# Optimization experiments

Hardware: AMD Instinct MI355X
Metric: run time of the kernel (lower is better)

Reference implementation:

```python
import jax, jax.numpy as jnp
import numpy as np

D_MODEL = 1024
N_HEADS = 4
KEY_DIM = 1024   # expand_k=1.0
VALUE_DIM = 2048 # expand_v=2.0
DK = KEY_DIM // N_HEADS    # 256
DV = VALUE_DIM // N_HEADS  # 512
LOW_RANK = 16
GATE_NORM = 16.0
EPS = 1e-5


def setup_inputs() -> dict:
    key = jax.random.key(0)
    ks = jax.random.split(key, 10)
    B, L = 2, 2048
    gain = 2.0 ** (-2.5)

    def xavier(k, shape, g=gain):
        fan_in, fan_out = shape[0], shape[1]
        a = g * np.sqrt(6.0 / (fan_in + fan_out))
        return jax.random.uniform(k, shape, jnp.float32, -a, a)

    return {
        "x": jax.random.normal(ks[0], (B, L, D_MODEL), jnp.float32),
        "Wq": xavier(ks[1], (D_MODEL, KEY_DIM)),
        "Wk": xavier(ks[2], (D_MODEL, KEY_DIM)),
        "Wv": xavier(ks[3], (D_MODEL, VALUE_DIM)),
        "Wg": xavier(ks[4], (D_MODEL, VALUE_DIM)),
        "gk_w1": xavier(ks[5], (D_MODEL, LOW_RANK)),
        "gk_w2": xavier(ks[6], (LOW_RANK, KEY_DIM)),
        "gk_b2": jnp.zeros((KEY_DIM,), jnp.float32),
        "g_norm_w": jnp.ones((DV,), jnp.float32),
        "Wo": xavier(ks[7], (VALUE_DIM, D_MODEL)),
    }


def _gla_scan(q, k, v, gk):
    # q,k: [B,H,L,Dk]; v: [B,H,L,Dv]; gk: [B,H,L,Dk] (log decay)
    # recurrence: S_t = diag(exp(gk_t)) S_{t-1} + k_t v_t^T ; o_t = q_t S_t
    B, H, L, dk = q.shape
    dv = v.shape[-1]
    # time-major for scan
    qs = jnp.moveaxis(q, 2, 0)
    ks_ = jnp.moveaxis(k, 2, 0)
    vs = jnp.moveaxis(v, 2, 0)
    gs = jnp.moveaxis(gk, 2, 0)

    def step(S, inp):
        q_t, k_t, v_t, g_t = inp  # [B,H,Dk], [B,H,Dk], [B,H,Dv], [B,H,Dk]
        S = S * jnp.exp(g_t)[..., None] + k_t[..., None] * v_t[..., None, :]
        o_t = jnp.einsum('bhk,bhkv->bhv', q_t, S)
        return S, o_t

    S0 = jnp.zeros((B, H, dk, dv), q.dtype)
    _, os = jax.lax.scan(step, S0, (qs, ks_, vs, gs))
    return jnp.moveaxis(os, 0, 2)  # [B,H,L,Dv]


def reference(x, Wq, Wk, Wv, Wg, gk_w1, gk_w2, gk_b2, g_norm_w, Wo):
    B, L, _ = x.shape
    scale = DK ** -0.5

    def heads(t, d):
        return t.reshape(B, L, N_HEADS, d).transpose(0, 2, 1, 3)  # b h l d

    q = heads(x @ Wq, DK) * scale
    k = heads(x @ Wk, DK)
    v = heads(x @ Wv, DV)
    gk = heads(jax.nn.log_sigmoid((x @ gk_w1) @ gk_w2 + gk_b2) / GATE_NORM, DK)

    o = _gla_scan(q, k, v, gk)                 # [B,H,L,Dv]
    o = o.transpose(0, 2, 1, 3)                # [B,L,H,Dv]

    g = (x @ Wg).reshape(B, L, N_HEADS, DV)
    # FusedRMSNormSwishGate: RMSNorm(o) * silu(g)
    rms = o * jax.lax.rsqrt(jnp.mean(o * o, axis=-1, keepdims=True) + EPS)
    o = (rms * g_norm_w) * (g * jax.nn.sigmoid(g))
    o = o.reshape(B, L, VALUE_DIM)
    return o @ Wo
```

## Files before the change

### kernel.cpp

```cpp
#include <hip/hip_runtime.h>
#include <hip/hip_bf16.h>
#include <math.h>

#define NHEADS 4
#define DKH 256
#define DVH 512
#define SEQL 2048
#define NB 2
#define NTOK (NB*SEQL)
#define DM 1024
#define KDT 1024
#define VDT 2048
#define CHUNK 128
#define NCH (SEQL/CHUNK)

typedef unsigned short u16;
typedef unsigned int   u32;
typedef unsigned long long u64;
typedef __attribute__((ext_vector_type(8))) short bf16x8;
typedef __attribute__((ext_vector_type(4))) float f32x4;

__device__ inline u16 f2bf(float f) {
  __hip_bfloat16 h = __float2bfloat16(f);
  return *reinterpret_cast<u16*>(&h);
}
__device__ inline float bf2f(u16 u) {
  u32 x = ((u32)u) << 16;
  return __uint_as_float(x);
}

__device__ __forceinline__ void gload16(const u16* g, u16* l) {
  __builtin_amdgcn_global_load_lds(
      (const __attribute__((address_space(1))) u32*)g,
      (__attribute__((address_space(3))) u32*)l,
      16, 0, 0);
}

__global__ __launch_bounds__(256)
void f2bf_kernel(const float* __restrict__ in, u16* __restrict__ out, int n)
{
  const int i = (blockIdx.x * 256 + threadIdx.x) * 8;
  if (i >= n) return;
  const float4 x0 = *(const float4*)&in[i];
  const float4 x1 = *(const float4*)&in[i + 4];
  int4 p;
  p.x = f2bf(x0.x) | ((u32)f2bf(x0.y) << 16);
  p.y = f2bf(x0.z) | ((u32)f2bf(x0.w) << 16);
  p.z = f2bf(x1.x) | ((u32)f2bf(x1.y) << 16);
  p.w = f2bf(x1.z) | ((u32)f2bf(x1.w) << 16);
  *(int4*)&out[i] = p;
}

__global__ __launch_bounds__(256)
void transpose_f2bf(const float* __restrict__ W, u16* __restrict__ Wt, int K, int N)
{
  __shared__ float Ts[64][69];
  const int n0 = blockIdx.x * 64, k0 = blockIdx.y * 64;
  const int tx = threadIdx.x & 15, ty = threadIdx.x >> 4;
  #pragma unroll
  for (int r = 0; r < 4; ++r) {
    const int k = ty + r * 16;
    const float4 w4 = *(const float4*)&W[(size_t)(k0 + k) * N + n0 + tx * 4];
    Ts[tx*4 + 0][k] = w4.x;
    Ts[tx*4 + 1][k] = w4.y;
    Ts[tx*4 + 2][k] = w4.z;
    Ts[tx*4 + 3][k] = w4.w;
  }
  __syncthreads();
  #pragma unroll
  for (int r = 0; r < 4; ++r) {
    const int n = ty + r * 16;
    u64 pk = (u64)f2bf(Ts[n][tx*4 + 0]) | ((u64)f2bf(Ts[n][tx*4 + 1]) << 16)
           | ((u64)f2bf(Ts[n][tx*4 + 2]) << 32) | ((u64)f2bf(Ts[n][tx*4 + 3]) << 48);
    *(u64*)&Wt[(size_t)(n0 + n) * K + k0 + tx * 4] = pk;
  }
}

__global__ __launch_bounds__(256)
void gemm_qkvg(const u16* __restrict__ A, const u16* __restrict__ Wall,
               u16* __restrict__ Qh, u16* __restrict__ Kh,
               u16* __restrict__ Vt, u16* __restrict__ Gh, float qscale)
{
  __shared__ __align__(16) u16 As[2][128 * 32];
  __shared__ __align__(16) u16 Bs[2][128 * 32];
  const int tid = threadIdx.x;
  const int lane = tid & 63, wave = tid >> 6;
  const int wr = wave >> 1, wc = wave & 1;
  const int l15 = lane & 15, l4 = lane >> 4;
  const int bx = blockIdx.x;
  const int bm = blockIdx.y * 128, bn = bx * 128;

  f32x4 acc[4][4];
  #pragma unroll
  for (int i = 0; i < 4; ++i)
    #pragma unroll
    for (int j = 0; j < 4; ++j)
      acc[i][j] = (f32x4){0.f, 0.f, 0.f, 0.f};

  const int sRow = wave * 32 + (lane >> 2);
  const int sCol = (lane & 3) * 8;
  const u16* Ag0 = &A   [(size_t)(bm + sRow) * DM + sCol];
  const u16* Ag1 = &A   [(size_t)(bm + sRow + 16) * DM + sCol];
  const u16* Bg0 = &Wall[(size_t)(bn + sRow) * DM + sCol];
  const u16* Bg1 = &Wall[(size_t)(bn + sRow + 16) * DM + sCol];
  const int lb0 = (wave * 32) * 32, lb1 = (wave * 32 + 16) * 32;

  gload16(Ag0, &As[0][lb0]);
  gload16(Ag1, &As[0][lb1]);
  gload16(Bg0, &Bs[0][lb0]);
  gload16(Bg1, &Bs[0][lb1]);
  __syncthreads();

  for (int k0 = 0; k0 < DM; k0 += 32) {
    const int cur = (k0 >> 5) & 1;
    if (k0 + 32 < DM) {
      gload16(Ag0 + k0 + 32, &As[cur ^ 1][lb0]);
      gload16(Ag1 + k0 + 32, &As[cur ^ 1][lb1]);
      gload16(Bg0 + k0 + 32, &Bs[cur ^ 1][lb0]);
      gload16(Bg1 + k0 + 32, &Bs[cur ^ 1][lb1]);
    }
    bf16x8 af[4], bfv[4];
    #pragma unroll
    for (int mi = 0; mi < 4; ++mi)
      af[mi] = *(const bf16x8*)&As[cur][(wr*64 + mi*16 + l15) * 32 + l4*8];
    #pragma unroll
    for (int ni = 0; ni < 4; ++ni)
      bfv[ni] = *(const bf16x8*)&Bs[cur][(wc*64 + ni*16 + l15) * 32 + l4*8];
    #pragma unroll
    for (int mi = 0; mi < 4; ++mi)
      #pragma unroll
      for (int ni = 0; ni < 4; ++ni)
        acc[mi][ni] = __builtin_amdgcn_mfma_f32_16x16x32_bf16(af[mi], bfv[ni], acc[mi][ni], 0, 0, 0);
    __syncthreads();
  }

  if (bx < 8) {
    #pragma unroll
    for (int mi = 0; mi < 4; ++mi)
      #pragma unroll
      for (int ni = 0; ni < 4; ++ni) {
        const int col = bn + wc*64 + ni*16 + l15;
        #pragma unroll
        for (int r = 0; r < 4; ++r)
          Qh[(size_t)(bm + wr*64 + mi*16 + l4*4 + r) * 1024 + col] = f2bf(acc[mi][ni][r] * qscale);
      }
  } else if (bx < 16) {
    #pragma unroll
    for (int mi = 0; mi < 4; ++mi)
      #pragma unroll
      for (int ni = 0; ni < 4; ++ni) {
        const int col = bn - 1024 + wc*64 + ni*16 + l15;
        #pragma unroll
        for (int r = 0; r < 4; ++r)
          Kh[(size_t)(bm + wr*64 + mi*16 + l4*4 + r) * 1024 + col] = f2bf(acc[mi][ni][r]);
      }
  } else if (bx < 32) {
    #pragma unroll
    for (int mi = 0; mi < 4; ++mi) {
      const int row0 = bm + wr*64 + mi*16 + l4*4;
      const int b = row0 >> 11, l = row0 & 2047;
      #pragma unroll
      for (int ni = 0; ni < 4; ++ni) {
        const int colV = bn - 2048 + wc*64 + ni*16 + l15;
        const int h = colV >> 9, dv = colV & 511;
        u64 pk = (u64)f2bf(acc[mi][ni][0]) | ((u64)f2bf(acc[mi][ni][1]) << 16)
               | ((u64)f2bf(acc[mi][ni][2]) << 32) | ((u64)f2bf(acc[mi][ni][3]) << 48);
        *(u64*)&Vt[((size_t)((b*4 + h)*512 + dv)) * SEQL + l] = pk;
      }
    }
  } else {
    #pragma unroll
    for (int mi = 0; mi < 4; ++mi)
      #pragma unroll
      for (int ni = 0; ni < 4; ++ni) {
        const int col = bn - 4096 + wc*64 + ni*16 + l15;
        #pragma unroll
        for (int r = 0; r < 4; ++r)
          Gh[(size_t)(bm + wr*64 + mi*16 + l4*4 + r) * 2048 + col] = f2bf(acc[mi][ni][r]);
      }
  }
}

__global__ __launch_bounds__(256)
void gemm_bf16(const u16* __restrict__ A, const u16* __restrict__ Bt,
               float* __restrict__ C, int M, int N, int K, float scale)
{
  __shared__ __align__(16) u16 As[2][128 * 32];
  __shared__ __align__(16) u16 Bs[2][128 * 32];
  const int tid = threadIdx.x;
  const int lane = tid & 63, wave = tid >> 6;
  const int wr = wave >> 1, wc = wave & 1;
  const int l15 = lane & 15, l4 = lane >> 4;
  const int bm = blockIdx.y * 128, bn = blockIdx.x * 128;

  f32x4 acc[4][4];
  #pragma unroll
  for (int i = 0; i < 4; ++i)
    #pragma unroll
    for (int j = 0; j < 4; ++j)
      acc[i][j] = (f32x4){0.f, 0.f, 0.f, 0.f};

  const int sRow = wave * 32 + (lane >> 2);
  const int sCol = (lane & 3) * 8;
  const u16* Ag0 = &A [(size_t)(bm + sRow) * K + sCol];
  const u16* Ag1 = &A [(size_t)(bm + sRow + 16) * K + sCol];
  const u16* Bg0 = &Bt[(size_t)(bn + sRow) * K + sCol];
  const u16* Bg1 = &Bt[(size_t)(bn + sRow + 16) * K + sCol];
  const int lb0 = (wave * 32) * 32, lb1 = (wave * 32 + 16) * 32;

  gload16(Ag0, &As[0][lb0]);
  gload16(Ag1, &As[0][lb1]);
  gload16(Bg0, &Bs[0][lb0]);
  gload16(Bg1, &Bs[0][lb1]);
  __syncthreads();

  for (int k0 = 0; k0 < K; k0 += 32) {
    const int cur = (k0 >> 5) & 1;
    if (k0 + 32 < K) {
      gload16(Ag0 + k0 + 32, &As[cur ^ 1][lb0]);
      gload16(Ag1 + k0 + 32, &As[cur ^ 1][lb1]);
      gload16(Bg0 + k0 + 32, &Bs[cur ^ 1][lb0]);
      gload16(Bg1 + k0 + 32, &Bs[cur ^ 1][lb1]);
    }
    bf16x8 af[4], bfv[4];
    #pragma unroll
    for (int mi = 0; mi < 4; ++mi)
      af[mi] = *(const bf16x8*)&As[cur][(wr*64 + mi*16 + l15) * 32 + l4*8];
    #pragma unroll
    for (int ni = 0; ni < 4; ++ni)
      bfv[ni] = *(const bf16x8*)&Bs[cur][(wc*64 + ni*16 + l15) * 32 + l4*8];
    #pragma unroll
    for (int mi = 0; mi < 4; ++mi)
      #pragma unroll
      for (int ni = 0; ni < 4; ++ni)
        acc[mi][ni] = __builtin_amdgcn_mfma_f32_16x16x32_bf16(af[mi], bfv[ni], acc[mi][ni], 0, 0, 0);
    __syncthreads();
  }

  #pragma unroll
  for (int mi = 0; mi < 4; ++mi)
    #pragma unroll
    for (int ni = 0; ni < 4; ++ni) {
      const int col = bn + wc*64 + ni*16 + l15;
      #pragma unroll
      for (int r = 0; r < 4; ++r) {
        const int row = bm + wr*64 + mi*16 + l4*4 + r;
        C[(size_t)row * N + col] = acc[mi][ni][r] * scale;
      }
    }
}

__global__ __launch_bounds__(256)
void gemm_u(const float* __restrict__ X, const float* __restrict__ W1,
            float* __restrict__ U)
{
  __shared__ float Xs[64][65];
  __shared__ __align__(16) float W1s[64][16];
  const int tid = threadIdx.x;
  const int row0 = blockIdx.x * 64;
  const int rr = tid & 63, gg = tid >> 6;
  float acc[4] = {0.f, 0.f, 0.f, 0.f};
  for (int k0 = 0; k0 < DM; k0 += 64) {
    #pragma unroll
    for (int rep = 0; rep < 4; ++rep) {
      const int m = (tid >> 4) + rep * 16;
      const int kk = (tid & 15) << 2;
      const float4 x4 = *(const float4*)&X[(size_t)(row0 + m) * DM + k0 + kk];
      Xs[kk+0][m] = x4.x; Xs[kk+1][m] = x4.y; Xs[kk+2][m] = x4.z; Xs[kk+3][m] = x4.w;
    }
    {
      const int kk = tid >> 2, n = (tid & 3) << 2;
      *(float4*)&W1s[kk][n] = *(const float4*)&W1[(size_t)(k0 + kk) * 16 + n];
    }
    __syncthreads();
    #pragma unroll
    for (int k2 = 0; k2 < 64; ++k2) {
      const float xv = Xs[k2][rr];
      const float4 w4 = *(const float4*)&W1s[k2][gg << 2];
      acc[0] += xv * w4.x; acc[1] += xv * w4.y; acc[2] += xv * w4.z; acc[3] += xv * w4.w;
    }
    __syncthreads();
  }
  *(float4*)&U[(size_t)(row0 + rr) * 16 + (gg << 2)] =
      make_float4(acc[0], acc[1], acc[2], acc[3]);
}

__device__ inline float ls_exp(float z) {
  const float ls = (z >= 0.f) ? -log1pf(expf(-z)) : (z - log1pf(expf(z)));
  return expf(ls * 0.0625f);
}

__global__ __launch_bounds__(256)
void gate_kernel(const float* __restrict__ U, const float* __restrict__ W2,
                 const float* __restrict__ b2, float* __restrict__ EGKo)
{
  __shared__ float Us[16];
  const int row = blockIdx.x, tid = threadIdx.x;
  if (tid < 16) Us[tid] = U[row * 16 + tid];
  __syncthreads();
  const int d0 = tid << 2;
  float4 z = *(const float4*)&b2[d0];
  #pragma unroll
  for (int r = 0; r < 16; ++r) {
    const float u = Us[r];
    const float4 w4 = *(const float4*)&W2[r * 1024 + d0];
    z.x += u * w4.x; z.y += u * w4.y; z.z += u * w4.z; z.w += u * w4.w;
  }
  float4 e = make_float4(ls_exp(z.x), ls_exp(z.y), ls_exp(z.z), ls_exp(z.w));
  *(float4*)&EGKo[(size_t)row * 1024 + d0] = e;
}

__global__ __launch_bounds__(256)
void chunk_prep(const u16* __restrict__ Qh, const u16* __restrict__ Kh,
                const float* __restrict__ EG, u16* __restrict__ qtb,
                u16* __restrict__ ktb, u16* __restrict__ khb,
                float* __restrict__ lamC)
{
  const int j = blockIdx.x;
  const int bh = blockIdx.y;
  const int b = bh >> 2, h = bh & 3;
  const int tid = threadIdx.x;
  const size_t base = ((size_t)(b * SEQL + j * CHUNK)) * KDT + h * DKH + tid;
  float cum = 1.f;
  for (int t = 0; t < CHUNK; t += 4) {
    const size_t i0 = base + (size_t)t * KDT;
    float d[4], q[4], k[4];
    #pragma unroll
    for (int u = 0; u < 4; ++u) {
      d[u] = EG[i0 + (size_t)u * KDT];
      q[u] = bf2f(Qh[i0 + (size_t)u * KDT]);
      k[u] = bf2f(Kh[i0 + (size_t)u * KDT]);
    }
    #pragma unroll
    for (int u = 0; u < 4; ++u) {
      cum *= d[u];
      qtb[i0 + (size_t)u * KDT] = f2bf(q[u] * cum);
      ktb[i0 + (size_t)u * KDT] = f2bf(k[u] / cum);
    }
  }
  lamC[(bh * NCH + j) * 256 + tid] = cum;
  for (int t = 0; t < CHUNK; t += 4) {
    const size_t i0 = base + (size_t)t * KDT;
    u16 kt4[4];
    #pragma unroll
    for (int u = 0; u < 4; ++u) kt4[u] = ktb[i0 + (size_t)u * KDT];
    #pragma unroll
    for (int u = 0; u < 4; ++u)
      khb[i0 + (size_t)u * KDT] = f2bf(bf2f(kt4[u]) * cum);
  }
}

__global__ __launch_bounds__(256)
void gla_pstate_mfma(const u16* __restrict__ kh, const u16* __restrict__ Vt,
                     float* __restrict__ P)
{
  const int mb = blockIdx.x, nb = blockIdx.y, jc = blockIdx.z;
  const int bh = jc >> 4, j = jc & 15;
  const int b = bh >> 2, h = bh & 3;
  const int tid = threadIdx.x;
  const int lane = tid & 63, wave = tid >> 6;
  const int wr = wave >> 1, wc = wave & 1;
  const int l15 = lane & 15, l4 = lane >> 4;
  const int tok0 = b * SEQL + j * CHUNK;

  __shared__ __align__(16) u16 Al[128 * 40];
  __shared__ __align__(16) u16 Blt[128 * 40];

  f32x4 acc[4][4];
  #pragma unroll
  for (int i = 0; i < 4; ++i)
    #pragma unroll
    for (int jj = 0; jj < 4; ++jj) acc[i][jj] = (f32x4){0.f,0.f,0.f,0.f};

  for (int kt0 = 0; kt0 < CHUNK; kt0 += 32) {
    {
      const int srow = tid >> 2, scol = (tid & 3) * 8;
      *(int4*)&Al[(srow)    * 40 + scol] =
        *(const int4*)&Vt[((size_t)(bh*512 + mb*128 + srow))    * SEQL + j*CHUNK + kt0 + scol];
      *(int4*)&Al[(64+srow) * 40 + scol] =
        *(const int4*)&Vt[((size_t)(bh*512 + mb*128 + 64+srow)) * SEQL + j*CHUNK + kt0 + scol];
    }
    {
      const int t = tid & 31;
      #pragma unroll
      for (int i = 0; i < 2; ++i) {
        const int dkg = (tid >> 5) * 16 + i * 8;
        int4 v = *(const int4*)&kh[(size_t)(tok0 + kt0 + t) * KDT + h*DKH + nb*128 + dkg];
        const u16* pv = (const u16*)&v;
        #pragma unroll
        for (int u = 0; u < 8; ++u) Blt[(dkg + u)*40 + t] = pv[u];
      }
    }
    __syncthreads();
    bf16x8 af[4], bv[4];
    #pragma unroll
    for (int mi = 0; mi < 4; ++mi)
      af[mi] = *(const bf16x8*)&Al[(wr*64 + mi*16 + l15)*40 + l4*8];
    #pragma unroll
    for (int ni = 0; ni < 4; ++ni)
      bv[ni] = *(const bf16x8*)&Blt[(wc*64 + ni*16 + l15)*40 + l4*8];
    #pragma unroll
    for (int mi = 0; mi < 4; ++mi)
      #pragma unroll
      for (int ni = 0; ni < 4; ++ni)
        acc[mi][ni] = __builtin_amdgcn_mfma_f32_16x16x32_bf16(af[mi], bv[ni], acc[mi][ni], 0, 0, 0);
    __syncthreads();
  }

  #pragma unroll
  for (int mi = 0; mi < 4; ++mi)
    #pragma unroll
    for (int ni = 0; ni < 4; ++ni) {
      const int col = nb*128 + wc*64 + ni*16 + l15;
      #pragma unroll
      for (int r = 0; r < 4; ++r) {
        const int row = mb*128 + wr*64 + mi*16 + l4*4 + r;
        P[(size_t)jc * 131072 + (size_t)row * 256 + col] = acc[mi][ni][r];
      }
    }
}

__global__ __launch_bounds__(256)
void gla_sscan(const float* __restrict__ P, const float* __restrict__ lamC,
               u16* __restrict__ SjT)
{
  const int bh = blockIdx.y;
  const int e0 = blockIdx.x * 1024 + threadIdx.x * 4;
  const int dv = e0 >> 8, dk = e0 & 255;
  float4 S = make_float4(0.f, 0.f, 0.f, 0.f);
  for (int j = 0; j < NCH; ++j) {
    const size_t cb = (size_t)(bh * NCH + j);
    const float4 lam = *(const float4*)&lamC[cb * 256 + dk];
    const size_t idx = cb * 131072 + (size_t)dv * 256 + dk;
    const float4 tmp = *(const float4*)&P[idx];
    u64 pk = (u64)f2bf(S.x) | ((u64)f2bf(S.y) << 16)
           | ((u64)f2bf(S.z) << 32) | ((u64)f2bf(S.w) << 48);
    *(u64*)&SjT[idx] = pk;
    S.x = lam.x * S.x + tmp.x;
    S.y = lam.y * S.y + tmp.y;
    S.z = lam.z * S.z + tmp.z;
    S.w = lam.w * S.w + tmp.w;
  }
}

__global__ __launch_bounds__(256)
void gla_intra_mfma(const u16* __restrict__ qt, const u16* __restrict__ kt,
                    const u16* __restrict__ Vt, const u16* __restrict__ SjT,
                    float* __restrict__ O)
{
  const int half = blockIdx.x;
  const int j    = blockIdx.y;
  const int bh   = blockIdx.z;
  const int b = bh >> 2, h = bh & 3;
  const int tid = threadIdx.x;
  const int lane = tid & 63, wave = tid >> 6;
  const int wr = wave >> 1, wc = wave & 1;
  const int l15 = lane & 15, l4 = lane >> 4;
  const int tok0 = b * SEQL + j * CHUNK;

  __shared__ __align__(16) u16 Pl[128 * 136];
  __shared__ __align__(16) u16 stg[128 * 136];
  u16* As = stg;
  u16* Bs = stg + 128 * 40;

  const size_t qkBase = (size_t)tok0 * KDT + h * DKH;
  const size_t sjBase = (size_t)(bh * NCH + j) * 131072;

  const int srow = tid >> 2;
  const int scol = (tid & 3) * 8;

  f32x4 acc[4][4];
  #pragma unroll
  for (int i = 0; i < 4; ++i)
    #pragma unroll
    for (int jj = 0; jj < 4; ++jj) acc[i][jj] = (f32x4){0.f,0.f,0.f,0.f};

  int4 ra0 = *(const int4*)&qt[qkBase + (size_t)srow      * KDT + scol];
  int4 ra1 = *(const int4*)&qt[qkBase + (size_t)(64+srow) * KDT + scol];
  int4 rb0 = *(const int4*)&kt[qkBase + (size_t)srow      * KDT + scol];
  int4 rb1 = *(const int4*)&kt[qkBase + (size_t)(64+srow) * KDT + scol];

  for (int dk0 = 0; dk0 < DKH; dk0 += 32) {
    __syncthreads();
    *(int4*)&As[(srow)    * 40 + scol] = ra0;
    *(int4*)&As[(64+srow) * 40 + scol] = ra1;
    *(int4*)&Bs[(srow)    * 40 + scol] = rb0;
    *(int4*)&Bs[(64+srow) * 40 + scol] = rb1;
    __syncthreads();
    if (dk0 + 32 < DKH) {
      ra0 = *(const int4*)&qt[qkBase + (size_t)srow      * KDT + dk0 + 32 + scol];
      ra1 = *(const int4*)&qt[qkBase + (size_t)(64+srow) * KDT + dk0 + 32 + scol];
      rb0 = *(const int4*)&kt[qkBase + (size_t)srow      * KDT + dk0 + 32 + scol];
      rb1 = *(const int4*)&kt[qkBase + (size_t)(64+srow) * KDT + dk0 + 32 + scol];
    }
    bf16x8 af[4], bv[4];
    #pragma unroll
    for (int mi = 0; mi < 4; ++mi)
      af[mi] = *(const bf16x8*)&As[(wr*64 + mi*16 + l15) * 40 + l4*8];
    #pragma unroll
    for (int ni = 0; ni < 4; ++ni)
      bv[ni] = *(const bf16x8*)&Bs[(wc*64 + ni*16 + l15) * 40 + l4*8];
    #pragma unroll
    for (int mi = 0; mi < 4; ++mi)
      #pragma unroll
      for (int ni = 0; ni < 4; ++ni)
        acc[mi][ni] = __builtin_amdgcn_mfma_f32_16x16x32_bf16(af[mi], bv[ni], acc[mi][ni], 0, 0, 0);
  }
  __syncthreads();

  #pragma unroll
  for (int mi = 0; mi < 4; ++mi)
    #pragma unroll
    for (int ni = 0; ni < 4; ++ni) {
      const int s = wc*64 + ni*16 + l15;
      #pragma unroll
      for (int r = 0; r < 4; ++r) {
        const int t = wr*64 + mi*16 + l4*4 + r;
        Pl[t*136 + s] = (s <= t) ? f2bf(acc[mi][ni][r]) : (u16)0;
      }
    }
  __syncthreads();

  for (int dt = 0; dt < 2; ++dt) {
    const int dvBase = half*256 + dt*128;
    f32x4 acc2[4][4];
    #pragma unroll
    for (int i = 0; i < 4; ++i)
      #pragma unroll
      for (int jj = 0; jj < 4; ++jj) acc2[i][jj] = (f32x4){0.f,0.f,0.f,0.f};

    int4 ia0 = *(const int4*)&qt [qkBase + (size_t)srow      * KDT + scol];
    int4 ia1 = *(const int4*)&qt [qkBase + (size_t)(64+srow) * KDT + scol];
    int4 ib0 = *(const int4*)&SjT[sjBase + (size_t)(dvBase + srow)      * 256 + scol];
    int4 ib1 = *(const int4*)&SjT[sjBase + (size_t)(dvBase + 64 + srow) * 256 + scol];

    for (int k0 = 0; k0 < DKH; k0 += 32) {
      __syncthreads();
      *(int4*)&As[(srow)    * 40 + scol] = ia0;
      *(int4*)&As[(64+srow) * 40 + scol] = ia1;
      *(int4*)&Bs[(srow)    * 40 + scol] = ib0;
      *(int4*)&Bs[(64+srow) * 40 + scol] = ib1;
      __syncthreads();
      if (k0 + 32 < DKH) {
        ia0 = *(const int4*)&qt [qkBase + (size_t)srow      * KDT + k0 + 32 + scol];
        ia1 = *(const int4*)&qt [qkBase + (size_t)(64+srow) * KDT + k0 + 32 + scol];
        ib0 = *(const int4*)&SjT[sjBase + (size_t)(dvBase + srow)      * 256 + k0 + 32 + scol];
        ib1 = *(const int4*)&SjT[sjBase + (size_t)(dvBase + 64 + srow) * 256 + k0 + 32 + scol];
      }
      bf16x8 af[4], bv[4];
      #pragma unroll
      for (int mi = 0; mi < 4; ++mi)
        af[mi] = *(const bf16x8*)&As[(wr*64 + mi*16 + l15) * 40 + l4*8];
      #pragma unroll
      for (int ni = 0; ni < 4; ++ni)
        bv[ni] = *(const bf16x8*)&Bs[(wc*64 + ni*16 + l15) * 40 + l4*8];
      #pragma unroll
      for (int mi = 0; mi < 4; ++mi)
        #pragma unroll
        for (int ni = 0; ni < 4; ++ni)
          acc2[mi][ni] = __builtin_amdgcn_mfma_f32_16x16x32_bf16(af[mi], bv[ni], acc2[mi][ni], 0, 0, 0);
    }
    __syncthreads();

    #pragma unroll
    for (int i = 0; i < 8; ++i) {
      const int row = i*16 + (tid >> 4);
      const int col8 = (tid & 15) * 8;
      *(int4*)&stg[row*136 + col8] =
        *(const int4*)&Vt[((size_t)(bh*512 + dvBase + row)) * SEQL + j*CHUNK + col8];
    }
    __syncthreads();
    #pragma unroll
    for (int ks = 0; ks < 4; ++ks) {
      bf16x8 af2[4], bv2[4];
      #pragma unroll
      for (int mi = 0; mi < 4; ++mi)
        af2[mi] = *(const bf16x8*)&Pl[(wr*64 + mi*16 + l15)*136 + ks*32 + l4*8];
      #pragma unroll
      for (int ni = 0; ni < 4; ++ni)
        bv2[ni] = *(const bf16x8*)&stg[(wc*64 + ni*16 + l15)*136 + ks*32 + l4*8];
      #pragma unroll
      for (int mi = 0; mi < 4; ++mi)
        #pragma unroll
        for (int ni = 0; ni < 4; ++ni)
          acc2[mi][ni] = __builtin_amdgcn_mfma_f32_16x16x32_bf16(af2[mi], bv2[ni], acc2[mi][ni], 0, 0, 0);
    }
    #pragma unroll
    for (int mi = 0; mi < 4; ++mi)
      #pragma unroll
      for (int ni = 0; ni < 4; ++ni) {
        const int col = h*DVH + dvBase + wc*64 + ni*16 + l15;
        #pragma unroll
        for (int r = 0; r < 4; ++r) {
          const int row = tok0 + wr*64 + mi*16 + l4*4 + r;
          O[(size_t)row * VDT + col] = acc2[mi][ni][r];
        }
      }
    __syncthreads();
  }
}

__global__ __launch_bounds__(256)
void epilogue(const float* __restrict__ O, const u16* __restrict__ G,
              const float* __restrict__ w, u16* __restrict__ Y)
{
  const int row = blockIdx.x;
  const int tid = threadIdx.x;
  __shared__ float sred[4];
  for (int h = 0; h < NHEADS; ++h) {
    const size_t base = (size_t)row * VDT + h * DVH;
    const float2 o2 = *(const float2*)&O[base + tid * 2];
    float ss = o2.x * o2.x + o2.y * o2.y;
    #pragma unroll
    for (int off = 32; off > 0; off >>= 1) ss += __shfl_down(ss, off);
    if ((tid & 63) == 0) sred[tid >> 6] = ss;
    __syncthreads();
    const float tot = sred[0] + sred[1] + sred[2] + sred[3];
    const float rs = rsqrtf(tot * (1.f / DVH) + 1e-5f);
    const u32 g2p = *(const u32*)&G[base + tid * 2];
    const float gx = bf2f((u16)(g2p & 0xffff));
    const float gy = bf2f((u16)(g2p >> 16));
    const float2 w2 = *(const float2*)&w[tid * 2];
    const float y0 = o2.x * rs * w2.x * gx / (1.f + expf(-gx));
    const float y1 = o2.y * rs * w2.y * gy / (1.f + expf(-gy));
    const u32 pk = (u32)f2bf(y0) | ((u32)f2bf(y1) << 16);
    *(u32*)&Y[base + tid * 2] = pk;
    __syncthreads();
  }
}

extern "C" void kernel_launch(void* const* d_in, const int* in_sizes, int n_in,
                              void* d_out, int out_size, void* d_ws, size_t ws_size,
                              hipStream_t stream)
{
  const float* x    = (const float*)d_in[0];
  const float* Wq   = (const float*)d_in[1];
  const float* Wk   = (const float*)d_in[2];
  const float* Wv   = (const float*)d_in[3];
  const float* Wg   = (const float*)d_in[4];
  const float* gw1  = (const float*)d_in[5];
  const float* gw2  = (const float*)d_in[6];
  const float* gb2  = (const float*)d_in[7];
  const float* gnw  = (const float*)d_in[8];
  const float* Wo   = (const float*)d_in[9];
  float* out = (float*)d_out;

  float* ws = (float*)d_ws;
  const size_t M = 1024ull * 1024ull;
  u16*   Qbh  = (u16*)(ws);
  u16*   Kbh  = (u16*)(ws + 2*M);
  float* EGK  = ws + 4*M;
  u16*   Vtb  = (u16*)(ws + 8*M);
  u16*   qtb  = (u16*)(ws + 12*M);
  u16*   ktb  = (u16*)(ws + 14*M);
  u16*   Gbh  = (u16*)(ws + 16*M);
  float* Ob   = ws + 20*M;
  float* Sjb  = ws + 28*M;
  float* lamC = ws + 44*M;
  float* Ub   = ws + 44*M + 32768;
  u16*   khb  = (u16*)(ws + 45*M);
  u16*   xb   = (u16*)(ws + 47*M);
  u16*   Wallb= (u16*)(ws + 49*M);
  u16*   Wob  = (u16*)(ws + 52*M);
  u16*   SjTb = (u16*)(ws + 53*M);
  u16*   Y2b  = (u16*)(ws);

  const float qscale = 0.0625f;

  f2bf_kernel  <<<2048, 256, 0, stream>>>(x, xb, NTOK * DM);
  transpose_f2bf<<<dim3(16, 16), 256, 0, stream>>>(Wq, Wallb,                1024, 1024);
  transpose_f2bf<<<dim3(16, 16), 256, 0, stream>>>(Wk, Wallb + 1024*1024,    1024, 1024);
  transpose_f2bf<<<dim3(32, 16), 256, 0, stream>>>(Wv, Wallb + 2048*1024,    1024, 2048);
  transpose_f2bf<<<dim3(32, 16), 256, 0, stream>>>(Wg, Wallb + 4096ull*1024, 1024, 2048);
  transpose_f2bf<<<dim3(16, 32), 256, 0, stream>>>(Wo, Wob, 2048, 1024);

  gemm_qkvg<<<dim3(48, 32), 256, 0, stream>>>(xb, Wallb, Qbh, Kbh, Vtb, Gbh, qscale);
  gemm_u      <<<64, 256, 0, stream>>>(x, gw1, Ub);
  gate_kernel <<<NTOK, 256, 0, stream>>>(Ub, gw2, gb2, EGK);

  chunk_prep<<<dim3(NCH, 8), 256, 0, stream>>>(Qbh, Kbh, EGK, qtb, ktb, khb, lamC);

  gla_pstate_mfma<<<dim3(4, 2, 128), 256, 0, stream>>>(khb, Vtb, Sjb);
  gla_sscan      <<<dim3(128, 8), 256, 0, stream>>>(Sjb, lamC, SjTb);
  gla_intra_mfma <<<dim3(2, NCH, 8), 256, 0, stream>>>(qtb, ktb, Vtb, SjTb, Ob);

  epilogue<<<NTOK, 256, 0, stream>>>(Ob, Gbh, gnw, Y2b);
  gemm_bf16<<<dim3(8, 32), 256, 0, stream>>>(Y2b, Wob, out, NTOK, 1024, 2048, 1.f);
}
```

Measured before the change: 301.3 us.

## Widen QKVG GEMM tile to 128x256 with swizzle and fuse intra q·S passes

The fused QKVG projection GEMM moves from 128x128 to 128x256 tiles, so each wave holds 4x8 accumulators and the grid halves. A block-index remap groups tiles that share A rows. In the intra-chunk kernel, the two q·S_j inter-chunk products for both 128-wide dv halves are now computed in one k-loop that shares the q tile, rather than reloading q for each half. This halves redundant q loads and raises MFMA work per LDS read, at the cost of roughly double accumulator registers, which may lower occupancy or cause spills.

```diff
diff --git a/kernel.cpp b/kernel.cpp
--- a/kernel.cpp
+++ b/kernel.cpp
@@ -82,86 +82,94 @@
                u16* __restrict__ Vt, u16* __restrict__ Gh, float qscale)
 {
   __shared__ __align__(16) u16 As[2][128 * 32];
-  __shared__ __align__(16) u16 Bs[2][128 * 32];
+  __shared__ __align__(16) u16 Bs[2][256 * 32];
   const int tid = threadIdx.x;
   const int lane = tid & 63, wave = tid >> 6;
   const int wr = wave >> 1, wc = wave & 1;
   const int l15 = lane & 15, l4 = lane >> 4;
-  const int bx = blockIdx.x;
-  const int bm = blockIdx.y * 128, bn = bx * 128;
-
-  f32x4 acc[4][4];
+
+  const int flat = blockIdx.y * 24 + blockIdx.x;
+  const int nf = (flat & 7) * 96 + (flat >> 3);
+  const int bx = nf % 24, by = nf / 24;
+  const int bm = by * 128, bn = bx * 256;
+
+  f32x4 acc[4][8];
   #pragma unroll
   for (int i = 0; i < 4; ++i)
     #pragma unroll
-    for (int j = 0; j < 4; ++j)
+    for (int j = 0; j < 8; ++j)
       acc[i][j] = (f32x4){0.f, 0.f, 0.f, 0.f};
 
-  const int sRow = wave * 32 + (lane >> 2);
-  const int sCol = (lane & 3) * 8;
-  const u16* Ag0 = &A   [(size_t)(bm + sRow) * DM + sCol];
-  const u16* Ag1 = &A   [(size_t)(bm + sRow + 16) * DM + sCol];
-  const u16* Bg0 = &Wall[(size_t)(bn + sRow) * DM + sCol];
-  const u16* Bg1 = &Wall[(size_t)(bn + sRow + 16) * DM + sCol];
-  const int lb0 = (wave * 32) * 32, lb1 = (wave * 32 + 16) * 32;
-
-  gload16(Ag0, &As[0][lb0]);
-  gload16(Ag1, &As[0][lb1]);
-  gload16(Bg0, &Bs[0][lb0]);
-  gload16(Bg1, &Bs[0][lb1]);
+  const int sR = lane >> 2;
+  const int sC = (lane & 3) * 8;
+  const u16* Ag0 = &A[(size_t)(bm + wave*32 + sR) * DM + sC];
+  const u16* Ag1 = &A[(size_t)(bm + wave*32 + 16 + sR) * DM + sC];
+  const u16* Bg[4];
+  #pragma unroll
+  for (int q = 0; q < 4; ++q)
+    Bg[q] = &Wall[(size_t)(bn + wave*64 + q*16 + sR) * DM + sC];
+  const int la0 = (wave*32) * 32, la1 = (wave*32 + 16) * 32;
+  int lb[4];
+  #pragma unroll
+  for (int q = 0; q < 4; ++q) lb[q] = (wave*64 + q*16) * 32;
+
+  gload16(Ag0, &As[0][la0]);
+  gload16(Ag1, &As[0][la1]);
+  #pragma unroll
+  for (int q = 0; q < 4; ++q) gload16(Bg[q], &Bs[0][lb[q]]);
   __syncthreads();
 
   for (int k0 = 0; k0 < DM; k0 += 32) {
     const int cur = (k0 >> 5) & 1;
     if (k0 + 32 < DM) {
-      gload16(Ag0 + k0 + 32, &As[cur ^ 1][lb0]);
-      gload16(Ag1 + k0 + 32, &As[cur ^ 1][lb1]);
-      gload16(Bg0 + k0 + 32, &Bs[cur ^ 1][lb0]);
-      gload16(Bg1 + k0 + 32, &Bs[cur ^ 1][lb1]);
-    }
-    bf16x8 af[4], bfv[4];
+      gload16(Ag0 + k0 + 32, &As[cur ^ 1][la0]);
+      gload16(Ag1 + k0 + 32, &As[cur ^ 1][la1]);
+      #pragma unroll
+      for (int q = 0; q < 4; ++q) gload16(Bg[q] + k0 + 32, &Bs[cur ^ 1][lb[q]]);
+    }
+    bf16x8 af[4], bfv[8];
     #pragma unroll
     for (int mi = 0; mi < 4; ++mi)
       af[mi] = *(const bf16x8*)&As[cur][(wr*64 + mi*16 + l15) * 32 + l4*8];
     #pragma unroll
-    for (int ni = 0; ni < 4; ++ni)
-      bfv[ni] = *(const bf16x8*)&Bs[cur][(wc*64 + ni*16 + l15) * 32 + l4*8];
-    #pragma unroll
-    for (int mi = 0; mi < 4; ++mi)
-      #pragma unroll
-      for (int ni = 0; ni < 4; ++ni)
+    for (int ni = 0; ni < 8; ++ni)
+      bfv[ni] = *(const bf16x8*)&Bs[cur][(wc*128 + ni*16 + l15) * 32 + l4*8];
+    #pragma unroll
+    for (int mi = 0; mi < 4; ++mi)
+      #pragma unroll
+      for (int ni = 0; ni < 8; ++ni)
         acc[mi][ni] = __builtin_amdgcn_mfma_f32_16x16x32_bf16(af[mi], bfv[ni], acc[mi][ni], 0, 0, 0);
     __syncthreads();
   }
 
-  if (bx < 8) {
-    #pragma unroll
-    for (int mi = 0; mi < 4; ++mi)
-      #pragma unroll
-      for (int ni = 0; ni < 4; ++ni) {
-        const int col = bn + wc*64 + ni*16 + l15;
+  if (bx < 4) {
+    #pragma unroll
+    for (int mi = 0; mi < 4; ++mi)
+      #pragma unroll
+      for (int ni = 0; ni < 8; ++ni) {
+        const int col = bn + wc*128 + ni*16 + l15;
         #pragma unroll
         for (int r = 0; r < 4; ++r)
           Qh[(size_t)(bm + wr*64 + mi*16 + l4*4 + r) * 1024 + col] = f2bf(acc[mi][ni][r] * qscale);
       }
-  } else if (bx < 16) {
-    #pragma unroll
-    for (int mi = 0; mi < 4; ++mi)
-      #pragma unroll
-      for (int ni = 0; ni < 4; ++ni) {
-        const int col = bn - 1024 + wc*64 + ni*16 + l15;
+  } else if (bx < 8) {
+    #pragma unroll
+    for (int mi = 0; mi < 4; ++mi)
+      #pragma unroll
+      for (int ni = 0; ni < 8; ++ni) {
+        const int col = bn - 1024 + wc*128 + ni*16 + l15;
         #pragma unroll
         for (int r = 0; r < 4; ++r)
           Kh[(size_t)(bm + wr*64 + mi*16 + l4*4 + r) * 1024 + col] = f2bf(acc[mi][ni][r]);
       }
-  } else if (bx < 32) {
+  } else if (bx < 16) {
     #pragma unroll
     for (int mi = 0; mi < 4; ++mi) {
       const int row0 = bm + wr*64 + mi*16 + l4*4;
       const int b = row0 >> 11, l = row0 & 2047;
       #pragma unroll
-      for (int ni = 0; ni < 4; ++ni) {
-        const int colV = bn - 2048 + wc*64 + ni*16 + l15;
+      for (int ni = 0; ni < 8; ++ni) {
+        const int colV = bn - 2048 + wc*128 + ni*16 + l15;
         const int h = colV >> 9, dv = colV & 511;
         u64 pk = (u64)f2bf(acc[mi][ni][0]) | ((u64)f2bf(acc[mi][ni][1]) << 16)
                | ((u64)f2bf(acc[mi][ni][2]) << 32) | ((u64)f2bf(acc[mi][ni][3]) << 48);
@@ -172,8 +180,8 @@
     #pragma unroll
     for (int mi = 0; mi < 4; ++mi)
       #pragma unroll
-      for (int ni = 0; ni < 4; ++ni) {
-        const int col = bn - 4096 + wc*64 + ni*16 + l15;
+      for (int ni = 0; ni < 8; ++ni) {
+        const int col = bn - 4096 + wc*128 + ni*16 + l15;
         #pragma unroll
         for (int r = 0; r < 4; ++r)
           Gh[(size_t)(bm + wr*64 + mi*16 + l4*4 + r) * 2048 + col] = f2bf(acc[mi][ni][r]);
@@ -460,8 +468,9 @@
 
   __shared__ __align__(16) u16 Pl[128 * 136];
   __shared__ __align__(16) u16 stg[128 * 136];
-  u16* As = stg;
-  u16* Bs = stg + 128 * 40;
+  u16* As  = stg;
+  u16* Bs0 = stg + 128 * 40;
+  u16* Bs1 = stg + 2 * 128 * 40;
 
   const size_t qkBase = (size_t)tok0 * KDT + h * DKH;
   const size_t sjBase = (size_t)(bh * NCH + j) * 131072;
@@ -482,10 +491,10 @@
 
   for (int dk0 = 0; dk0 < DKH; dk0 += 32) {
     __syncthreads();
-    *(int4*)&As[(srow)    * 40 + scol] = ra0;
-    *(int4*)&As[(64+srow) * 40 + scol] = ra1;
-    *(int4*)&Bs[(srow)    * 40 + scol] = rb0;
-    *(int4*)&Bs[(64+srow) * 40 + scol] = rb1;
+    *(int4*)&As [(srow)    * 40 + scol] = ra0;
+    *(int4*)&As [(64+srow) * 40 + scol] = ra1;
+    *(int4*)&Bs0[(srow)    * 40 + scol] = rb0;
+    *(int4*)&Bs0[(64+srow) * 40 + scol] = rb1;
     __syncthreads();
     if (dk0 + 32 < DKH) {
       ra0 = *(const int4*)&qt[qkBase + (size_t)srow      * KDT + dk0 + 32 + scol];
@@ -499,7 +508,7 @@
       af[mi] = *(const bf16x8*)&As[(wr*64 + mi*16 + l15) * 40 + l4*8];
     #pragma unroll
     for (int ni = 0; ni < 4; ++ni)
-      bv[ni] = *(const bf16x8*)&Bs[(wc*64 + ni*16 + l15) * 40 + l4*8];
+      bv[ni] = *(const bf16x8*)&Bs0[(wc*64 + ni*16 + l15) * 40 + l4*8];
     #pragma unroll
     for (int mi = 0; mi < 4; ++mi)
       #pragma unroll
@@ -521,47 +530,61 @@
     }
   __syncthreads();
 
+  const int dv0 = half*256;
+  const int dv1 = half*256 + 128;
+  f32x4 acc2[2][4][4];
+  #pragma unroll
+  for (int d = 0; d < 2; ++d)
+    #pragma unroll
+    for (int i = 0; i < 4; ++i)
+      #pragma unroll
+      for (int jj = 0; jj < 4; ++jj) acc2[d][i][jj] = (f32x4){0.f,0.f,0.f,0.f};
+
+  int4 ia0 = *(const int4*)&qt [qkBase + (size_t)srow      * KDT + scol];
+  int4 ia1 = *(const int4*)&qt [qkBase + (size_t)(64+srow) * KDT + scol];
+  int4 ib0 = *(const int4*)&SjT[sjBase + (size_t)(dv0 + srow)      * 256 + scol];
+  int4 ib1 = *(const int4*)&SjT[sjBase + (size_t)(dv0 + 64 + srow) * 256 + scol];
+  int4 ic0 = *(const int4*)&SjT[sjBase + (size_t)(dv1 + srow)      * 256 + scol];
+  int4 ic1 = *(const int4*)&SjT[sjBase + (size_t)(dv1 + 64 + srow) * 256 + scol];
+
+  for (int k0 = 0; k0 < DKH; k0 += 32) {
+    __syncthreads();
+    *(int4*)&As [(srow)    * 40 + scol] = ia0;
+    *(int4*)&As [(64+srow) * 40 + scol] = ia1;
+    *(int4*)&Bs0[(srow)    * 40 + scol] = ib0;
+    *(int4*)&Bs0[(64+srow) * 40 + scol] = ib1;
+    *(int4*)&Bs1[(srow)    * 40 + scol] = ic0;
+    *(int4*)&Bs1[(64+srow) * 40 + scol] = ic1;
+    __syncthreads();
+    if (k0 + 32 < DKH) {
+      ia0 = *(const int4*)&qt [qkBase + (size_t)srow      * KDT + k0 + 32 + scol];
+      ia1 = *(const int4*)&qt [qkBase + (size_t)(64+srow) * KDT + k0 + 32 + scol];
+      ib0 = *(const int4*)&SjT[sjBase + (size_t)(dv0 + srow)      * 256 + k0 + 32 + scol];
+      ib1 = *(const int4*)&SjT[sjBase + (size_t)(dv0 + 64 + srow) * 256 + k0 + 32 + scol];
+      ic0 = *(const int4*)&SjT[sjBase + (size_t)(dv1 + srow)      * 256 + k0 + 32 + scol];
+      ic1 = *(const int4*)&SjT[sjBase + (size_t)(dv1 + 64 + srow) * 256 + k0 + 32 + scol];
+    }
+    bf16x8 af[4], bv0[4], bv1[4];
+    #pragma unroll
+    for (int mi = 0; mi < 4; ++mi)
+      af[mi] = *(const bf16x8*)&As[(wr*64 + mi*16 + l15) * 40 + l4*8];
+    #pragma unroll
+    for (int ni = 0; ni < 4; ++ni) {
+      bv0[ni] = *(const bf16x8*)&Bs0[(wc*64 + ni*16 + l15) * 40 + l4*8];
+      bv1[ni] = *(const bf16x8*)&Bs1[(wc*64 + ni*16 + l15) * 40 + l4*8];
+    }
+    #pragma unroll
+    for (int mi = 0; mi < 4; ++mi)
+      #pragma unroll
+      for (int ni = 0; ni < 4; ++ni) {
+        acc2[0][mi][ni] = __builtin_amdgcn_mfma_f32_16x16x32_bf16(af[mi], bv0[ni], acc2[0][mi][ni], 0, 0, 0);
+        acc2[1][mi][ni] = __builtin_amdgcn_mfma_f32_16x16x32_bf16(af[mi], bv1[ni], acc2[1][mi][ni], 0, 0, 0);
+      }
+  }
+  __syncthreads();
+
   for (int dt = 0; dt < 2; ++dt) {
     const int dvBase = half*256 + dt*128;
-    f32x4 acc2[4][4];
-    #pragma unroll
-    for (int i = 0; i < 4; ++i)
-      #pragma unroll
-      for (int jj = 0; jj < 4; ++jj) acc2[i][jj] = (f32x4){0.f,0.f,0.f,0.f};
-
-    int4 ia0 = *(const int4*)&qt [qkBase + (size_t)srow      * KDT + scol];
-    int4 ia1 = *(const int4*)&qt [qkBase + (size_t)(64+srow) * KDT + scol];
-    int4 ib0 = *(const int4*)&SjT[sjBase + (size_t)(dvBase + srow)      * 256 + scol];
-    int4 ib1 = *(const int4*)&SjT[sjBase + (size_t)(dvBase + 64 + srow) * 256 + scol];
-
-    for (int k0 = 0; k0 < DKH; k0 += 32) {
-      __syncthreads();
-      *(int4*)&As[(srow)    * 40 + scol] = ia0;
-      *(int4*)&As[(64+srow) * 40 + scol] = ia1;
-      *(int4*)&Bs[(srow)    * 40 + scol] = ib0;
-      *(int4*)&Bs[(64+srow) * 40 + scol] = ib1;
-      __syncthreads();
-      if (k0 + 32 < DKH) {
-        ia0 = *(const int4*)&qt [qkBase + (size_t)srow      * KDT + k0 + 32 + scol];
-        ia1 = *(const int4*)&qt [qkBase + (size_t)(64+srow) * KDT + k0 + 32 + scol];
-        ib0 = *(const int4*)&SjT[sjBase + (size_t)(dvBase + srow)      * 256 + k0 + 32 + scol];
-        ib1 = *(const int4*)&SjT[sjBase + (size_t)(dvBase + 64 + srow) * 256 + k0 + 32 + scol];
-      }
-      bf16x8 af[4], bv[4];
-      #pragma unroll
-      for (int mi = 0; mi < 4; ++mi)
-        af[mi] = *(const bf16x8*)&As[(wr*64 + mi*16 + l15) * 40 + l4*8];
-      #pragma unroll
-      for (int ni = 0; ni < 4; ++ni)
-        bv[ni] = *(const bf16x8*)&Bs[(wc*64 + ni*16 + l15) * 40 + l4*8];
-      #pragma unroll
-      for (int mi = 0; mi < 4; ++mi)
-        #pragma unroll
-        for (int ni = 0; ni < 4; ++ni)
-          acc2[mi][ni] = __builtin_amdgcn_mfma_f32_16x16x32_bf16(af[mi], bv[ni], acc2[mi][ni], 0, 0, 0);
-    }
-    __syncthreads();
-
     #pragma unroll
     for (int i = 0; i < 8; ++i) {
       const int row = i*16 + (tid >> 4);
@@ -583,7 +606,7 @@
       for (int mi = 0; mi < 4; ++mi)
         #pragma unroll
         for (int ni = 0; ni < 4; ++ni)
-          acc2[mi][ni] = __builtin_amdgcn_mfma_f32_16x16x32_bf16(af2[mi], bv2[ni], acc2[mi][ni], 0, 0, 0);
+          acc2[dt][mi][ni] = __builtin_amdgcn_mfma_f32_16x16x32_bf16(af2[mi], bv2[ni], acc2[dt][mi][ni], 0, 0, 0);
     }
     #pragma unroll
     for (int mi = 0; mi < 4; ++mi)
@@ -593,7 +616,7 @@
         #pragma unroll
         for (int r = 0; r < 4; ++r) {
           const int row = tok0 + wr*64 + mi*16 + l4*4 + r;
-          O[(size_t)row * VDT + col] = acc2[mi][ni][r];
+          O[(size_t)row * VDT + col] = acc2[dt][mi][ni][r];
         }
       }
     __syncthreads();
@@ -674,7 +697,7 @@
   transpose_f2bf<<<dim3(32, 16), 256, 0, stream>>>(Wg, Wallb + 4096ull*1024, 1024, 2048);
   transpose_f2bf<<<dim3(16, 32), 256, 0, stream>>>(Wo, Wob, 2048, 1024);
 
-  gemm_qkvg<<<dim3(48, 32), 256, 0, stream>>>(xb, Wallb, Qbh, Kbh, Vtb, Gbh, qscale);
+  gemm_qkvg<<<dim3(24, 32), 256, 0, stream>>>(xb, Wallb, Qbh, Kbh, Vtb, Gbh, qscale);
   gemm_u      <<<64, 256, 0, stream>>>(x, gw1, Ub);
   gate_kernel <<<NTOK, 256, 0, stream>>>(Ub, gw2, gb2, EGK);
 
```

Result: slower. 336.3 us (+11.6%).

## Store per-chunk state contributions in bf16 and fuse inter-chunk Q·S passes

Applied to the files above, without the earlier changes.

The per-chunk state contribution P written by gla_pstate_mfma and read by gla_sscan is now stored as bf16 instead of fp32, which halves that intermediate traffic. In gla_intra_mfma, the two dv-halves of the q·S_j product are computed in a single k-loop with two B tiles and a doubled accumulator, so the q tile is loaded once instead of twice. This costs some precision on P before accumulation in the scan, plus higher register pressure (32 accumulators per thread) and more shared memory staging per iteration.

```diff
diff --git a/kernel.cpp b/kernel.cpp
--- a/kernel.cpp
+++ b/kernel.cpp
@@ -352,7 +352,7 @@
 
 __global__ __launch_bounds__(256)
 void gla_pstate_mfma(const u16* __restrict__ kh, const u16* __restrict__ Vt,
-                     float* __restrict__ P)
+                     u16* __restrict__ P)
 {
   const int mb = blockIdx.x, nb = blockIdx.y, jc = blockIdx.z;
   const int bh = jc >> 4, j = jc & 15;
@@ -415,13 +415,13 @@
       #pragma unroll
       for (int r = 0; r < 4; ++r) {
         const int row = mb*128 + wr*64 + mi*16 + l4*4 + r;
-        P[(size_t)jc * 131072 + (size_t)row * 256 + col] = acc[mi][ni][r];
-      }
-    }
-}
-
-__global__ __launch_bounds__(256)
-void gla_sscan(const float* __restrict__ P, const float* __restrict__ lamC,
+        P[(size_t)jc * 131072 + (size_t)row * 256 + col] = f2bf(acc[mi][ni][r]);
+      }
+    }
+}
+
+__global__ __launch_bounds__(256)
+void gla_sscan(const u16* __restrict__ P, const float* __restrict__ lamC,
                u16* __restrict__ SjT)
 {
   const int bh = blockIdx.y;
@@ -432,14 +432,18 @@
     const size_t cb = (size_t)(bh * NCH + j);
     const float4 lam = *(const float4*)&lamC[cb * 256 + dk];
     const size_t idx = cb * 131072 + (size_t)dv * 256 + dk;
-    const float4 tmp = *(const float4*)&P[idx];
+    const u64 pkin = *(const u64*)&P[idx];
+    const float t0 = bf2f((u16)(pkin       & 0xffff));
+    const float t1 = bf2f((u16)((pkin>>16) & 0xffff));
+    const float t2 = bf2f((u16)((pkin>>32) & 0xffff));
+    const float t3 = bf2f((u16)((pkin>>48) & 0xffff));
     u64 pk = (u64)f2bf(S.x) | ((u64)f2bf(S.y) << 16)
            | ((u64)f2bf(S.z) << 32) | ((u64)f2bf(S.w) << 48);
     *(u64*)&SjT[idx] = pk;
-    S.x = lam.x * S.x + tmp.x;
-    S.y = lam.y * S.y + tmp.y;
-    S.z = lam.z * S.z + tmp.z;
-    S.w = lam.w * S.w + tmp.w;
+    S.x = lam.x * S.x + t0;
+    S.y = lam.y * S.y + t1;
+    S.z = lam.z * S.z + t2;
+    S.w = lam.w * S.w + t3;
   }
 }
 
@@ -460,8 +464,9 @@
 
   __shared__ __align__(16) u16 Pl[128 * 136];
   __shared__ __align__(16) u16 stg[128 * 136];
-  u16* As = stg;
-  u16* Bs = stg + 128 * 40;
+  u16* As  = stg;
+  u16* Bs0 = stg + 128 * 40;
+  u16* Bs1 = stg + 2 * 128 * 40;
 
   const size_t qkBase = (size_t)tok0 * KDT + h * DKH;
   const size_t sjBase = (size_t)(bh * NCH + j) * 131072;
@@ -482,10 +487,10 @@
 
   for (int dk0 = 0; dk0 < DKH; dk0 += 32) {
     __syncthreads();
-    *(int4*)&As[(srow)    * 40 + scol] = ra0;
-    *(int4*)&As[(64+srow) * 40 + scol] = ra1;
-    *(int4*)&Bs[(srow)    * 40 + scol] = rb0;
-    *(int4*)&Bs[(64+srow) * 40 + scol] = rb1;
+    *(int4*)&As [(srow)    * 40 + scol] = ra0;
+    *(int4*)&As [(64+srow) * 40 + scol] = ra1;
+    *(int4*)&Bs0[(srow)    * 40 + scol] = rb0;
+    *(int4*)&Bs0[(64+srow) * 40 + scol] = rb1;
     __syncthreads();
     if (dk0 + 32 < DKH) {
       ra0 = *(const int4*)&qt[qkBase + (size_t)srow      * KDT + dk0 + 32 + scol];
@@ -499,7 +504,7 @@
       af[mi] = *(const bf16x8*)&As[(wr*64 + mi*16 + l15) * 40 + l4*8];
     #pragma unroll
     for (int ni = 0; ni < 4; ++ni)
-      bv[ni] = *(const bf16x8*)&Bs[(wc*64 + ni*16 + l15) * 40 + l4*8];
+      bv[ni] = *(const bf16x8*)&Bs0[(wc*64 + ni*16 + l15) * 40 + l4*8];
     #pragma unroll
     for (int mi = 0; mi < 4; ++mi)
       #pragma unroll
@@ -521,47 +526,61 @@
     }
   __syncthreads();
 
+  const int dv0 = half*256;
+  const int dv1 = half*256 + 128;
+  f32x4 acc2[2][4][4];
+  #pragma unroll
+  for (int d = 0; d < 2; ++d)
+    #pragma unroll
+    for (int i = 0; i < 4; ++i)
+      #pragma unroll
+      for (int jj = 0; jj < 4; ++jj) acc2[d][i][jj] = (f32x4){0.f,0.f,0.f,0.f};
+
+  int4 ia0 = *(const int4*)&qt [qkBase + (size_t)srow      * KDT + scol];
+  int4 ia1 = *(const int4*)&qt [qkBase + (size_t)(64+srow) * KDT + scol];
+  int4 ib0 = *(const int4*)&SjT[sjBase + (size_t)(dv0 + srow)      * 256 + scol];
+  int4 ib1 = *(const int4*)&SjT[sjBase + (size_t)(dv0 + 64 + srow) * 256 + scol];
+  int4 ic0 = *(const int4*)&SjT[sjBase + (size_t)(dv1 + srow)      * 256 + scol];
+  int4 ic1 = *(const int4*)&SjT[sjBase + (size_t)(dv1 + 64 + srow) * 256 + scol];
+
+  for (int k0 = 0; k0 < DKH; k0 += 32) {
+    __syncthreads();
+    *(int4*)&As [(srow)    * 40 + scol] = ia0;
+    *(int4*)&As [(64+srow) * 40 + scol] = ia1;
+    *(int4*)&Bs0[(srow)    * 40 + scol] = ib0;
+    *(int4*)&Bs0[(64+srow) * 40 + scol] = ib1;
+    *(int4*)&Bs1[(srow)    * 40 + scol] = ic0;
+    *(int4*)&Bs1[(64+srow) * 40 + scol] = ic1;
+    __syncthreads();
+    if (k0 + 32 < DKH) {
+      ia0 = *(const int4*)&qt [qkBase + (size_t)srow      * KDT + k0 + 32 + scol];
+      ia1 = *(const int4*)&qt [qkBase + (size_t)(64+srow) * KDT + k0 + 32 + scol];
+      ib0 = *(const int4*)&SjT[sjBase + (size_t)(dv0 + srow)      * 256 + k0 + 32 + scol];
+      ib1 = *(const int4*)&SjT[sjBase + (size_t)(dv0 + 64 + srow) * 256 + k0 + 32 + scol];
+      ic0 = *(const int4*)&SjT[sjBase + (size_t)(dv1 + srow)      * 256 + k0 + 32 + scol];
+      ic1 = *(const int4*)&SjT[sjBase + (size_t)(dv1 + 64 + srow) * 256 + k0 + 32 + scol];
+    }
+    bf16x8 af[4], bv0[4], bv1[4];
+    #pragma unroll
+    for (int mi = 0; mi < 4; ++mi)
+      af[mi] = *(const bf16x8*)&As[(wr*64 + mi*16 + l15) * 40 + l4*8];
+    #pragma unroll
+    for (int ni = 0; ni < 4; ++ni) {
+      bv0[ni] = *(const bf16x8*)&Bs0[(wc*64 + ni*16 + l15) * 40 + l4*8];
+      bv1[ni] = *(const bf16x8*)&Bs1[(wc*64 + ni*16 + l15) * 40 + l4*8];
+    }
+    #pragma unroll
+    for (int mi = 0; mi < 4; ++mi)
+      #pragma unroll
+      for (int ni = 0; ni < 4; ++ni) {
+        acc2[0][mi][ni] = __builtin_amdgcn_mfma_f32_16x16x32_bf16(af[mi], bv0[ni], acc2[0][mi][ni], 0, 0, 0);
+        acc2[1][mi][ni] = __builtin_amdgcn_mfma_f32_16x16x32_bf16(af[mi], bv1[ni], acc2[1][mi][ni], 0, 0, 0);
+      }
+  }
+  __syncthreads();
+
   for (int dt = 0; dt < 2; ++dt) {
     const int dvBase = half*256 + dt*128;
-    f32x4 acc2[4][4];
-    #pragma unroll
-    for (int i = 0; i < 4; ++i)
-      #pragma unroll
-      for (int jj = 0; jj < 4; ++jj) acc2[i][jj] = (f32x4){0.f,0.f,0.f,0.f};
-
-    int4 ia0 = *(const int4*)&qt [qkBase + (size_t)srow      * KDT + scol];
-    int4 ia1 = *(const int4*)&qt [qkBase + (size_t)(64+srow) * KDT + scol];
-    int4 ib0 = *(const int4*)&SjT[sjBase + (size_t)(dvBase + srow)      * 256 + scol];
-    int4 ib1 = *(const int4*)&SjT[sjBase + (size_t)(dvBase + 64 + srow) * 256 + scol];
-
-    for (int k0 = 0; k0 < DKH; k0 += 32) {
-      __syncthreads();
-      *(int4*)&As[(srow)    * 40 + scol] = ia0;
-      *(int4*)&As[(64+srow) * 40 + scol] = ia1;
-      *(int4*)&Bs[(srow)    * 40 + scol] = ib0;
-      *(int4*)&Bs[(64+srow) * 40 + scol] = ib1;
-      __syncthreads();
-      if (k0 + 32 < DKH) {
-        ia0 = *(const int4*)&qt [qkBase + (size_t)srow      * KDT + k0 + 32 + scol];
-        ia1 = *(const int4*)&qt [qkBase + (size_t)(64+srow) * KDT + k0 + 32 + scol];
-        ib0 = *(const int4*)&SjT[sjBase + (size_t)(dvBase + srow)      * 256 + k0 + 32 + scol];
-        ib1 = *(const int4*)&SjT[sjBase + (size_t)(dvBase + 64 + srow) * 256 + k0 + 32 + scol];
-      }
-      bf16x8 af[4], bv[4];
-      #pragma unroll
-      for (int mi = 0; mi < 4; ++mi)
-        af[mi] = *(const bf16x8*)&As[(wr*64 + mi*16 + l15) * 40 + l4*8];
-      #pragma unroll
-      for (int ni = 0; ni < 4; ++ni)
-        bv[ni] = *(const bf16x8*)&Bs[(wc*64 + ni*16 + l15) * 40 + l4*8];
-      #pragma unroll
-      for (int mi = 0; mi < 4; ++mi)
-        #pragma unroll
-        for (int ni = 0; ni < 4; ++ni)
-          acc2[mi][ni] = __builtin_amdgcn_mfma_f32_16x16x32_bf16(af[mi], bv[ni], acc2[mi][ni], 0, 0, 0);
-    }
-    __syncthreads();
-
     #pragma unroll
     for (int i = 0; i < 8; ++i) {
       const int row = i*16 + (tid >> 4);
@@ -583,7 +602,7 @@
       for (int mi = 0; mi < 4; ++mi)
         #pragma unroll
         for (int ni = 0; ni < 4; ++ni)
-          acc2[mi][ni] = __builtin_amdgcn_mfma_f32_16x16x32_bf16(af2[mi], bv2[ni], acc2[mi][ni], 0, 0, 0);
+          acc2[dt][mi][ni] = __builtin_amdgcn_mfma_f32_16x16x32_bf16(af2[mi], bv2[ni], acc2[dt][mi][ni], 0, 0, 0);
     }
     #pragma unroll
     for (int mi = 0; mi < 4; ++mi)
@@ -593,7 +612,7 @@
         #pragma unroll
         for (int r = 0; r < 4; ++r) {
           const int row = tok0 + wr*64 + mi*16 + l4*4 + r;
-          O[(size_t)row * VDT + col] = acc2[mi][ni][r];
+          O[(size_t)row * VDT + col] = acc2[dt][mi][ni][r];
         }
       }
     __syncthreads();
@@ -655,7 +674,7 @@
   u16*   ktb  = (u16*)(ws + 14*M);
   u16*   Gbh  = (u16*)(ws + 16*M);
   float* Ob   = ws + 20*M;
-  float* Sjb  = ws + 28*M;
+  u16*   Pjb  = (u16*)(ws + 28*M);
   float* lamC = ws + 44*M;
   float* Ub   = ws + 44*M + 32768;
   u16*   khb  = (u16*)(ws + 45*M);
@@ -680,8 +699,8 @@
 
   chunk_prep<<<dim3(NCH, 8), 256, 0, stream>>>(Qbh, Kbh, EGK, qtb, ktb, khb, lamC);
 
-  gla_pstate_mfma<<<dim3(4, 2, 128), 256, 0, stream>>>(khb, Vtb, Sjb);
-  gla_sscan      <<<dim3(128, 8), 256, 0, stream>>>(Sjb, lamC, SjTb);
+  gla_pstate_mfma<<<dim3(4, 2, 128), 256, 0, stream>>>(khb, Vtb, Pjb);
+  gla_sscan      <<<dim3(128, 8), 256, 0, stream>>>(Pjb, lamC, SjTb);
   gla_intra_mfma <<<dim3(2, NCH, 8), 256, 0, stream>>>(qtb, ktb, Vtb, SjTb, Ob);
 
   epilogue<<<NTOK, 256, 0, stream>>>(Ob, Gbh, gnw, Y2b);
```

Measured after the change: 289.8 us. 1.04x faster.
